# Optimization experiments

Measured on AMD Instinct MI355X. Metric: run time of the kernel, lower is better.

Reference implementation:

```python
import jax, jax.numpy as jnp
import numpy as np

M, N, E, B, J = 8192, 16384, 2097152, 8, 3
IMG, CH = 128, 1
BCLIP = 1.0  # rLayer B


def setup_inputs() -> dict:
    key = jax.random.key(0)
    ks = jax.random.split(key, 9)
    # ~E/M = 256 nnz per row -> scale vals so outputs stay O(1)
    A_vals = jax.random.normal(ks[0], (E,), jnp.float32) / 16.0
    A_rows = jax.random.randint(ks[1], (E,), 0, M, jnp.int32)
    A_cols = jax.random.randint(ks[2], (E,), 0, N, jnp.int32)
    z = jax.random.normal(ks[3], (B, N), jnp.float32)
    u = jax.random.normal(ks[4], (B, N), jnp.float32)
    y = jax.random.normal(ks[5], (B, M), jnp.float32)
    W1 = jax.random.normal(ks[6], (J, 3, 3, CH, 32), jnp.float32) * 0.05
    W2 = jax.random.normal(ks[7], (J, 3, 3, 32, 32), jnp.float32) * 0.05
    W3 = jax.random.normal(ks[8], (J, 3, 3, 32, CH), jnp.float32) * 0.05
    etas = jnp.full((J,), 1e-3, jnp.float32)
    return {"A_vals": A_vals, "A_rows": A_rows, "A_cols": A_cols,
            "z": z, "u": u, "y": y, "W1": W1, "W2": W2, "W3": W3, "etas": etas}


def _spmm_xAT(x, vals, rows, cols):
    """x (B,N) @ A^T -> (B,M), A in COO (rows in [0,M), cols in [0,N))."""
    contrib = x.T[cols] * vals[:, None]            # (E, B)
    return jax.ops.segment_sum(contrib, rows, num_segments=M).T


def _spmm_xA(x, vals, rows, cols):
    """x (B,M) @ A -> (B,N)."""
    contrib = x.T[rows] * vals[:, None]            # (E, B)
    return jax.ops.segment_sum(contrib, cols, num_segments=N).T


def _conv(x, w):
    return jax.lax.conv_general_dilated(
        x, w, window_strides=(1, 1), padding='SAME',
        dimension_numbers=('NHWC', 'HWIO', 'NHWC'))


def reference(A_vals, A_rows, A_cols, z, u, y, W1, W2, W3, etas):
    for j in range(J):
        # rLayer: ISTA gradient step with per-sample norm clipping (normalize=True)
        resid = y - _spmm_xAT(z * u, A_vals, A_rows, A_cols)      # (B, M)
        v = u * _spmm_xA(resid, A_vals, A_rows, A_cols)           # (B, N)
        v_norm = jnp.linalg.norm(v, axis=1, keepdims=True)        # (B, 1)
        v = v / jnp.maximum(1.0, v_norm / BCLIP)
        r = z - etas[j] * v
        # CNN prox: two relu convs + linear conv, no bias
        x = r.reshape(B, IMG, IMG, CH)
        x = jax.nn.relu(_conv(x, W1[j]))
        x = jax.nn.relu(_conv(x, W2[j]))
        x = _conv(x, W3[j])
        z = jax.nn.relu(r + x.reshape(B, N))                      # project=True
    return z
```

## Files before the change

### kernel.cpp

```cpp
#include <hip/hip_runtime.h>
#include <hip/hip_bf16.h>

#define Mdim 8192
#define Ndim 16384
#define Ennz 2097152
#define Bsz 8
#define Jit 3
#define IMG 128
#define RCAP 512
#define CCAP 256
#define PSTRIDE 270336
#define QSTRIDE 135168

typedef __attribute__((ext_vector_type(8))) short bf8_t;
typedef __attribute__((ext_vector_type(4))) float f4_t;

__device__ __forceinline__ short f2b(float f){
    __hip_bfloat16 h = __float2bfloat16(f);
    return *reinterpret_cast<short*>(&h);
}
__device__ __forceinline__ float bval(unsigned e){
    return __uint_as_float(e & 0xFFFF0000u);
}

__global__ void k_prep(const float* __restrict__ W2, const float* __restrict__ W3,
                       short* __restrict__ w2p, short* __restrict__ w3p,
                       int* bin_pos, int* cnts){
    int i = blockIdx.x*256 + threadIdx.x;
    if(i < 24) bin_pos[i] = 0;
    if(i < 24576) cnts[i] = 0;
    if(i < 27648){
        int j = i / 9216, idx = i - j*9216;
        int kk = idx >> 10, rem = idx & 1023;
        int ic = rem >> 5, oc = rem & 31;
        w2p[(size_t)j*11520 + (kk*32 + oc)*40 + ic] = f2b(W2[i]);
    }
    if(i < 864) w3p[i] = f2b(W3[i]);
}

__global__ __launch_bounds__(256) void k_part(const float* __restrict__ vals,
        const int* __restrict__ rows, const int* __restrict__ cols,
        int* bin_pos, uint2* __restrict__ Pst, uint2* __restrict__ Qst){
    __shared__ int cnt[24], off[24], gbase[24], start[24];
    __shared__ uint2 stage[4096];
    int t = threadIdx.x;
    if(t < 24) cnt[t] = 0;
    __syncthreads();
    int base = blockIdx.x * 2048;
    int r[8], c[8]; float v[8];
    #pragma unroll
    for(int k = 0; k < 8; k++){
        int e = base + k*256 + t;
        r[k] = rows[e]; c[k] = cols[e]; v[k] = vals[e];
        atomicAdd(&cnt[r[k] >> 10], 1);
        atomicAdd(&cnt[8 + (c[k] >> 10)], 1);
    }
    __syncthreads();
    if(t == 0){
        int s = 0;
        for(int q = 0; q < 8; q++){ start[q] = s; s += cnt[q]; }
        s = 2048;
        for(int q = 8; q < 24; q++){ start[q] = s; s += cnt[q]; }
    }
    if(t < 24) off[t] = 0;
    __syncthreads();
    if(t < 24) gbase[t] = atomicAdd(&bin_pos[t], cnt[t]);
    #pragma unroll
    for(int k = 0; k < 8; k++){
        int pb = r[k] >> 10;
        int p = atomicAdd(&off[pb], 1);
        stage[start[pb] + p] = make_uint2(((unsigned)(r[k] & 1023) << 14) | (unsigned)c[k],
                                          __float_as_uint(v[k]));
        int qb = 8 + (c[k] >> 10);
        int q = atomicAdd(&off[qb], 1);
        stage[start[qb] + q] = make_uint2(((unsigned)(c[k] & 1023) << 13) | (unsigned)r[k],
                                          __float_as_uint(v[k]));
    }
    __syncthreads();
    for(int q = 0; q < 8; q++){
        int len = cnt[q];
        uint2* dst = Pst + (size_t)q*PSTRIDE + gbase[q];
        for(int k = t; k < len; k += 256) dst[k] = stage[start[q] + k];
    }
    for(int q = 8; q < 24; q++){
        int len = cnt[q];
        uint2* dst = Qst + (size_t)(q-8)*QSTRIDE + gbase[q];
        for(int k = t; k < len; k += 256) dst[k] = stage[start[q] + k];
    }
}

__global__ __launch_bounds__(256) void k_scat(const uint2* __restrict__ Pst,
        const uint2* __restrict__ Qst, const int* __restrict__ bin_pos,
        int* row_cnt, int* col_cnt, unsigned* __restrict__ rp, unsigned* __restrict__ cp,
        const float* __restrict__ z_in, const float* __restrict__ u,
        float* __restrict__ z_cur, float* __restrict__ zu_T){
    __shared__ int cnt[1024], curs[1024];
    int t = threadIdx.x;
    int bid = blockIdx.x;
    if(bid >= 768){
        int i = (bid - 768)*256 + t;
        int n = i >> 3, b = i & 7;
        float z = z_in[b*Ndim + n];
        z_cur[b*Ndim + n] = z;
        zu_T[i] = z * u[b*Ndim + n];
        return;
    }
    if(bid < 256){
        int g = bid & 7, chunk = bid >> 3;
        int len = bin_pos[g];
        int s0 = (int)(((long long)chunk * len) >> 5);
        int s1 = (int)(((long long)(chunk+1) * len) >> 5);
        for(int i = t; i < 1024; i += 256) cnt[i] = 0;
        __syncthreads();
        const uint2* base = Pst + (size_t)g*PSTRIDE;
        for(int k = s0 + t; k < s1; k += 256)
            atomicAdd(&cnt[base[k].x >> 14], 1);
        __syncthreads();
        for(int i = t; i < 1024; i += 256)
            curs[i] = atomicAdd(&row_cnt[g*1024 + i], cnt[i]);
        __syncthreads();
        for(int k = s0 + t; k < s1; k += 256){
            uint2 e = base[k];
            int r_l = e.x >> 14;
            int slot = atomicAdd(&curs[r_l], 1);
            if(slot < RCAP)
                rp[(size_t)(g*1024 + r_l)*RCAP + slot] =
                    (((unsigned)(unsigned short)f2b(__uint_as_float(e.y))) << 16)
                    | (e.x & 0x3FFFu);
        }
    } else {
        int bc = bid - 256;
        int g = bc & 15, chunk = bc >> 4;
        int len = bin_pos[8 + g];
        int s0 = (int)(((long long)chunk * len) >> 5);
        int s1 = (int)(((long long)(chunk+1) * len) >> 5);
        for(int i = t; i < 1024; i += 256) cnt[i] = 0;
        __syncthreads();
        const uint2* base = Qst + (size_t)g*QSTRIDE;
        for(int k = s0 + t; k < s1; k += 256)
            atomicAdd(&cnt[base[k].x >> 13], 1);
        __syncthreads();
        for(int i = t; i < 1024; i += 256)
            curs[i] = atomicAdd(&col_cnt[g*1024 + i], cnt[i]);
        __syncthreads();
        for(int k = s0 + t; k < s1; k += 256){
            uint2 e = base[k];
            int c_l = e.x >> 13;
            int slot = atomicAdd(&curs[c_l], 1);
            if(slot < CCAP)
                cp[(size_t)(g*1024 + c_l)*CCAP + slot] =
                    (((unsigned)(unsigned short)f2b(__uint_as_float(e.y))) << 16)
                    | (e.x & 0x1FFFu);
        }
    }
}

__global__ void k_spmm1g(const unsigned* __restrict__ rp, const int* __restrict__ row_cnt,
                         const float* __restrict__ y, const float* __restrict__ zu_T,
                         float* __restrict__ resid_T, float* __restrict__ ssq){
    if(blockIdx.x == 0 && threadIdx.x < 8) ssq[threadIdx.x] = 0.f;
    int m = (blockIdx.x*256 + threadIdx.x) >> 6;
    int lane = threadIdx.x & 63;
    int n_nz = min(row_cnt[m], RCAP);
    int b = lane & 7, ks = lane >> 3;
    const unsigned* base = rp + (size_t)m*RCAP;
    float acc = 0.f;
    for(int k = ks*4; k < n_nz; k += 32){
        uint4 e = *(const uint4*)(base + k);
        float w0 = bval(e.x);
        float w1 = (k+1 < n_nz) ? bval(e.y) : 0.f;
        float w2 = (k+2 < n_nz) ? bval(e.z) : 0.f;
        float w3 = (k+3 < n_nz) ? bval(e.w) : 0.f;
        acc = fmaf(w0, zu_T[(e.x & 0x3FFFu)*8 + b], acc);
        acc = fmaf(w1, zu_T[(e.y & 0x3FFFu)*8 + b], acc);
        acc = fmaf(w2, zu_T[(e.z & 0x3FFFu)*8 + b], acc);
        acc = fmaf(w3, zu_T[(e.w & 0x3FFFu)*8 + b], acc);
    }
    acc += __shfl_xor(acc, 8);
    acc += __shfl_xor(acc, 16);
    acc += __shfl_xor(acc, 32);
    if(ks == 0)
        resid_T[m*8 + b] = y[b*Mdim + m] - acc;
}

__global__ void k_spmm2g(const unsigned* __restrict__ cp, const int* __restrict__ col_cnt,
                         const float* __restrict__ resid_T, float* __restrict__ v_T){
    int n = (blockIdx.x*256 + threadIdx.x) >> 6;
    int lane = threadIdx.x & 63;
    int n_nz = min(col_cnt[n], CCAP);
    int b = lane & 7, ks = lane >> 3;
    const unsigned* base = cp + (size_t)n*CCAP;
    float acc = 0.f;
    for(int k = ks*4; k < n_nz; k += 32){
        uint4 e = *(const uint4*)(base + k);
        float w0 = bval(e.x);
        float w1 = (k+1 < n_nz) ? bval(e.y) : 0.f;
        float w2 = (k+2 < n_nz) ? bval(e.z) : 0.f;
        float w3 = (k+3 < n_nz) ? bval(e.w) : 0.f;
        acc = fmaf(w0, resid_T[(e.x & 0x1FFFu)*8 + b], acc);
        acc = fmaf(w1, resid_T[(e.y & 0x1FFFu)*8 + b], acc);
        acc = fmaf(w2, resid_T[(e.z & 0x1FFFu)*8 + b], acc);
        acc = fmaf(w3, resid_T[(e.w & 0x1FFFu)*8 + b], acc);
    }
    acc += __shfl_xor(acc, 8);
    acc += __shfl_xor(acc, 16);
    acc += __shfl_xor(acc, 32);
    if(ks == 0)
        v_T[n*8 + b] = acc;
}

__global__ __launch_bounds__(256) void k_normp(const float* __restrict__ u,
                        const float* __restrict__ v_T, float* __restrict__ ssq){
    int t = threadIdx.x;
    float s = 0.f;
    #pragma unroll
    for(int c = 0; c < 4; c++){
        int idx = c*32768 + blockIdx.x*256 + t;
        int n = idx >> 3, b = idx & 7;
        float tv = u[b*Ndim + n] * v_T[idx];
        s = fmaf(tv, tv, s);
    }
    s += __shfl_xor(s, 8);
    s += __shfl_xor(s, 16);
    s += __shfl_xor(s, 32);
    if(((t & 63) >> 3) == 0) atomicAdd(&ssq[t & 7], s);
}

__global__ __launch_bounds__(256) void k_conv123(
        const float* __restrict__ z_cur, const float* __restrict__ u,
        const float* __restrict__ v_T, const float* __restrict__ ssq,
        const float* __restrict__ etas, const float* __restrict__ W1,
        const short* __restrict__ w2p, const short* __restrict__ w3p,
        int j, float* __restrict__ dst, float* __restrict__ zu_T){
    __shared__ short w2t[9*32*40];
    __shared__ short x1t[144*40];
    __shared__ short x2t[100*40];
    __shared__ float w1s[288];
    __shared__ short w3b[288];
    __shared__ float r14[196];
    int t = threadIdx.x;
    int blk = blockIdx.x;
    int bb = blk >> 8, tile = blk & 255;
    int oy0 = (tile >> 4)*8, ox0 = (tile & 15)*8;

    for(int idx = t; idx < 1440; idx += 256)
        ((uint4*)w2t)[idx] = ((const uint4*)(w2p + (size_t)j*11520))[idx];
    for(int idx = t; idx < 288; idx += 256){
        w1s[idx] = W1[j*288 + idx];
        w3b[idx] = w3p[j*288 + idx];
    }
    if(t < 196){
        int yy = t/14, xx = t%14;
        int gy = oy0 + yy - 3, gx = ox0 + xx - 3;
        float val = 0.f;
        if((unsigned)gy < 128u && (unsigned)gx < 128u){
            int n = gy*IMG + gx;
            int idx = bb*Ndim + n;
            float scale = etas[j] / fmaxf(1.0f, sqrtf(ssq[bb]));
            val = z_cur[idx] - scale * u[idx] * v_T[n*8 + bb];
        }
        r14[t] = val;
    }
    __syncthreads();

    for(int idx = t; idx < 2304; idx += 256){
        int ocp = idx & 15, p = idx >> 4;
        int py = p/12, px = p%12;
        int gy = oy0 + py - 2, gx = ox0 + px - 2;
        float a0 = 0.f, a1 = 0.f;
        if((unsigned)gy < 128u && (unsigned)gx < 128u){
            #pragma unroll
            for(int ky = 0; ky < 3; ky++)
                #pragma unroll
                for(int kx = 0; kx < 3; kx++){
                    float rv = r14[(py+ky)*14 + (px+kx)];
                    a0 = fmaf(rv, w1s[(ky*3+kx)*32 + 2*ocp],     a0);
                    a1 = fmaf(rv, w1s[(ky*3+kx)*32 + 2*ocp + 1], a1);
                }
            a0 = fmaxf(a0, 0.f); a1 = fmaxf(a1, 0.f);
        }
        unsigned pack = (unsigned short)f2b(a0) | ((unsigned)(unsigned short)f2b(a1) << 16);
        ((unsigned*)x1t)[p*20 + ocp] = pack;
    }
    __syncthreads();

    int wv = t >> 6, lane = t & 63, mm = lane & 15, q = lane >> 4;

    #pragma unroll
    for(int rnd = 0; rnd < 2; rnd++){
        int p = rnd*64 + wv*16 + mm;
        int pp = min(p, 99);
        int py2 = pp/10, px2 = pp%10;
        f4_t acc0 = {0.f,0.f,0.f,0.f}, acc1 = {0.f,0.f,0.f,0.f};
        #pragma unroll
        for(int kk = 0; kk < 9; kk++){
            int ky = kk/3, kx = kk%3;
            bf8_t a  = *(const bf8_t*)&x1t[((py2+ky)*12 + (px2+kx))*40 + q*8];
            bf8_t b0 = *(const bf8_t*)&w2t[(kk*32 + mm)*40 + q*8];
            bf8_t b1 = *(const bf8_t*)&w2t[(kk*32 + 16 + mm)*40 + q*8];
            acc0 = __builtin_amdgcn_mfma_f32_16x16x32_bf16(a, b0, acc0, 0, 0, 0);
            acc1 = __builtin_amdgcn_mfma_f32_16x16x32_bf16(a, b1, acc1, 0, 0, 0);
        }
        #pragma unroll
        for(int reg = 0; reg < 4; reg++){
            int pw = rnd*64 + wv*16 + q*4 + reg;
            if(pw < 100){
                int py = pw/10, px = pw%10;
                int gy = oy0 + py - 1, gx = ox0 + px - 1;
                bool in = ((unsigned)gy < 128u) && ((unsigned)gx < 128u);
                x2t[pw*40 + mm]      = in ? f2b(fmaxf(acc0[reg], 0.f)) : (short)0;
                x2t[pw*40 + mm + 16] = in ? f2b(fmaxf(acc1[reg], 0.f)) : (short)0;
            }
        }
    }
    __syncthreads();

    int p3 = wv*16 + mm;
    int py3 = p3 >> 3, px3 = p3 & 7;
    f4_t acc = {0.f,0.f,0.f,0.f};
    #pragma unroll
    for(int kk = 0; kk < 9; kk++){
        int ky = kk/3, kx = kk%3;
        bf8_t a = *(const bf8_t*)&x2t[((py3+ky)*10 + (px3+kx))*40 + q*8];
        bf8_t bf;
        #pragma unroll
        for(int jj = 0; jj < 8; jj++)
            bf[jj] = (mm == 0) ? w3b[kk*32 + q*8 + jj] : (short)0;
        acc = __builtin_amdgcn_mfma_f32_16x16x32_bf16(a, bf, acc, 0, 0, 0);
    }
    if(mm == 0){
        #pragma unroll
        for(int reg = 0; reg < 4; reg++){
            int po = wv*16 + q*4 + reg;
            int py = po >> 3, px = po & 7;
            int gy = oy0 + py, gx = ox0 + px;
            int n = gy*IMG + gx;
            int idx = bb*Ndim + n;
            float r = r14[(py+3)*14 + (px+3)];
            float znew = fmaxf(r + acc[reg], 0.f);
            dst[idx] = znew;
            zu_T[n*8 + bb] = znew * u[idx];
        }
    }
}

extern "C" void kernel_launch(void* const* d_in, const int* in_sizes, int n_in,
                              void* d_out, int out_size, void* d_ws, size_t ws_size,
                              hipStream_t stream){
    const float* A_vals = (const float*)d_in[0];
    const int* A_rows = (const int*)d_in[1];
    const int* A_cols = (const int*)d_in[2];
    const float* z_in = (const float*)d_in[3];
    const float* u    = (const float*)d_in[4];
    const float* y    = (const float*)d_in[5];
    const float* W1   = (const float*)d_in[6];
    const float* W2   = (const float*)d_in[7];
    const float* W3   = (const float*)d_in[8];
    const float* etas = (const float*)d_in[9];

    float* ws = (float*)d_ws;
    float* z_cur   = ws;  ws += Bsz*Ndim;
    float* zu_T    = ws;  ws += Ndim*8;
    float* v_T     = ws;  ws += Ndim*8;
    float* resid_T = ws;  ws += Mdim*8;
    float* ssq     = ws;  ws += 8;
    int*   bin_pos = (int*)ws; ws += 32;
    int*   row_cnt = (int*)ws; ws += Mdim;
    int*   col_cnt = (int*)ws; ws += Ndim;
    short* w2p     = (short*)ws; ws += 3*11520/2;
    short* w3p     = (short*)ws; ws += 3*288/2 + 8;
    unsigned* rp = (unsigned*)ws; ws += (size_t)Mdim*RCAP;
    unsigned* cp = (unsigned*)ws; ws += (size_t)Ndim*CCAP;
    uint2* Pst = (uint2*)ws;  ws += (size_t)8*PSTRIDE*2;
    uint2* Qst = (uint2*)ws;

    k_prep<<<108, 256, 0, stream>>>(W2, W3, w2p, w3p, bin_pos, row_cnt);
    k_part<<<Ennz/2048, 256, 0, stream>>>(A_vals, A_rows, A_cols, bin_pos, Pst, Qst);
    k_scat<<<1280, 256, 0, stream>>>(Pst, Qst, bin_pos, row_cnt, col_cnt, rp, cp,
                                     z_in, u, z_cur, zu_T);

    for(int j = 0; j < Jit; j++){
        k_spmm1g<<<Mdim/4, 256, 0, stream>>>(rp, row_cnt, y, zu_T, resid_T, ssq);
        k_spmm2g<<<Ndim/4, 256, 0, stream>>>(cp, col_cnt, resid_T, v_T);
        k_normp<<<128, 256, 0, stream>>>(u, v_T, ssq);
        float* dst = (j == Jit-1) ? (float*)d_out : z_cur;
        k_conv123<<<Bsz*256, 256, 0, stream>>>(z_cur, u, v_T, ssq, etas,
                                               W1, w2p, w3p, j, dst, zu_T);
    }
}
```

Before: 326.9 us.

## Fuse norm reduction into SpMM2 and loop conv tiles per block

The per-sample squared-norm reduction moves into the second SpMM kernel. Each block accumulates in LDS and atomically adds into 64 striped partial slots, which removes the separate k_normp launch and its reread of v_T. The conv kernel now processes 4 tiles per block (512 blocks instead of 2048), so the shared W2/W1/W3 weight staging and the partial-norm reduction are amortised across tiles. z is ping-ponged between two buffers so that reads of the source and writes of the next iterate never alias. The trade-off is fewer conv blocks, which may lower occupancy and latency hiding, and more contended LDS atomics in SpMM2.

```diff
diff --git a/kernel.cpp b/kernel.cpp
--- a/kernel.cpp
+++ b/kernel.cpp
@@ -157,8 +157,11 @@
 
 __global__ void k_spmm1g(const unsigned* __restrict__ rp, const int* __restrict__ row_cnt,
                          const float* __restrict__ y, const float* __restrict__ zu_T,
-                         float* __restrict__ resid_T, float* __restrict__ ssq){
-    if(blockIdx.x == 0 && threadIdx.x < 8) ssq[threadIdx.x] = 0.f;
+                         float* __restrict__ resid_T, float* __restrict__ ssq_part){
+    if(blockIdx.x == 0){
+        ssq_part[threadIdx.x] = 0.f;
+        ssq_part[256 + threadIdx.x] = 0.f;
+    }
     int m = (blockIdx.x*256 + threadIdx.x) >> 6;
     int lane = threadIdx.x & 63;
     int n_nz = min(row_cnt[m], RCAP);
@@ -184,9 +187,14 @@
 }
 
 __global__ void k_spmm2g(const unsigned* __restrict__ cp, const int* __restrict__ col_cnt,
-                         const float* __restrict__ resid_T, float* __restrict__ v_T){
-    int n = (blockIdx.x*256 + threadIdx.x) >> 6;
-    int lane = threadIdx.x & 63;
+                         const float* __restrict__ resid_T, const float* __restrict__ u,
+                         float* __restrict__ v_T, float* __restrict__ ssq_part){
+    __shared__ float sred[8];
+    int t = threadIdx.x;
+    if(t < 8) sred[t] = 0.f;
+    __syncthreads();
+    int n = (blockIdx.x*256 + t) >> 6;
+    int lane = t & 63;
     int n_nz = min(col_cnt[n], CCAP);
     int b = lane & 7, ks = lane >> 3;
     const unsigned* base = cp + (size_t)n*CCAP;
@@ -205,43 +213,31 @@
     acc += __shfl_xor(acc, 8);
     acc += __shfl_xor(acc, 16);
     acc += __shfl_xor(acc, 32);
-    if(ks == 0)
+    if(ks == 0){
         v_T[n*8 + b] = acc;
-}
-
-__global__ __launch_bounds__(256) void k_normp(const float* __restrict__ u,
-                        const float* __restrict__ v_T, float* __restrict__ ssq){
-    int t = threadIdx.x;
-    float s = 0.f;
-    #pragma unroll
-    for(int c = 0; c < 4; c++){
-        int idx = c*32768 + blockIdx.x*256 + t;
-        int n = idx >> 3, b = idx & 7;
-        float tv = u[b*Ndim + n] * v_T[idx];
-        s = fmaf(tv, tv, s);
-    }
-    s += __shfl_xor(s, 8);
-    s += __shfl_xor(s, 16);
-    s += __shfl_xor(s, 32);
-    if(((t & 63) >> 3) == 0) atomicAdd(&ssq[t & 7], s);
+        float uv = u[b*Ndim + n] * acc;
+        atomicAdd(&sred[b], uv*uv);
+    }
+    __syncthreads();
+    if(t < 8) atomicAdd(&ssq_part[(blockIdx.x & 63)*8 + t], sred[t]);
 }
 
 __global__ __launch_bounds__(256) void k_conv123(
-        const float* __restrict__ z_cur, const float* __restrict__ u,
-        const float* __restrict__ v_T, const float* __restrict__ ssq,
+        const float* __restrict__ z_src, const float* __restrict__ u,
+        const float* __restrict__ v_T, const float* __restrict__ ssq_part,
         const float* __restrict__ etas, const float* __restrict__ W1,
         const short* __restrict__ w2p, const short* __restrict__ w3p,
-        int j, float* __restrict__ dst, float* __restrict__ zu_T){
+        int j, float* __restrict__ z_dst, float* __restrict__ zu_T){
     __shared__ short w2t[9*32*40];
     __shared__ short x1t[144*40];
     __shared__ short x2t[100*40];
     __shared__ float w1s[288];
     __shared__ short w3b[288];
     __shared__ float r14[196];
+    __shared__ float sc_lds;
     int t = threadIdx.x;
     int blk = blockIdx.x;
-    int bb = blk >> 8, tile = blk & 255;
-    int oy0 = (tile >> 4)*8, ox0 = (tile & 15)*8;
+    int bb = blk >> 6, tgroup = blk & 63;
 
     for(int idx = t; idx < 1440; idx += 256)
         ((uint4*)w2t)[idx] = ((const uint4*)(w2p + (size_t)j*11520))[idx];
@@ -249,98 +245,112 @@
         w1s[idx] = W1[j*288 + idx];
         w3b[idx] = w3p[j*288 + idx];
     }
-    if(t < 196){
-        int yy = t/14, xx = t%14;
-        int gy = oy0 + yy - 3, gx = ox0 + xx - 3;
-        float val = 0.f;
-        if((unsigned)gy < 128u && (unsigned)gx < 128u){
-            int n = gy*IMG + gx;
-            int idx = bb*Ndim + n;
-            float scale = etas[j] / fmaxf(1.0f, sqrtf(ssq[bb]));
-            val = z_cur[idx] - scale * u[idx] * v_T[n*8 + bb];
-        }
-        r14[t] = val;
-    }
-    __syncthreads();
-
-    for(int idx = t; idx < 2304; idx += 256){
-        int ocp = idx & 15, p = idx >> 4;
-        int py = p/12, px = p%12;
-        int gy = oy0 + py - 2, gx = ox0 + px - 2;
-        float a0 = 0.f, a1 = 0.f;
-        if((unsigned)gy < 128u && (unsigned)gx < 128u){
+    if(t < 64){
+        float sv = ssq_part[t*8 + bb];
+        #pragma unroll
+        for(int off = 32; off > 0; off >>= 1) sv += __shfl_xor(sv, off);
+        if(t == 0) sc_lds = etas[j] / fmaxf(1.0f, sqrtf(sv));
+    }
+    __syncthreads();
+    float sc = sc_lds;
+
+    int wv = t >> 6, lane = t & 63, mm = lane & 15, q = lane >> 4;
+
+    for(int tt = 0; tt < 4; tt++){
+        int tile = tgroup*4 + tt;
+        int oy0 = (tile >> 4)*8, ox0 = (tile & 15)*8;
+
+        if(t < 196){
+            int yy = t/14, xx = t%14;
+            int gy = oy0 + yy - 3, gx = ox0 + xx - 3;
+            float val = 0.f;
+            if((unsigned)gy < 128u && (unsigned)gx < 128u){
+                int n = gy*IMG + gx;
+                int idx = bb*Ndim + n;
+                val = z_src[idx] - sc * u[idx] * v_T[n*8 + bb];
+            }
+            r14[t] = val;
+        }
+        __syncthreads();
+
+        for(int idx = t; idx < 2304; idx += 256){
+            int ocp = idx & 15, p = idx >> 4;
+            int py = p/12, px = p%12;
+            int gy = oy0 + py - 2, gx = ox0 + px - 2;
+            float a0 = 0.f, a1 = 0.f;
+            if((unsigned)gy < 128u && (unsigned)gx < 128u){
+                #pragma unroll
+                for(int ky = 0; ky < 3; ky++)
+                    #pragma unroll
+                    for(int kx = 0; kx < 3; kx++){
+                        float rv = r14[(py+ky)*14 + (px+kx)];
+                        a0 = fmaf(rv, w1s[(ky*3+kx)*32 + 2*ocp],     a0);
+                        a1 = fmaf(rv, w1s[(ky*3+kx)*32 + 2*ocp + 1], a1);
+                    }
+                a0 = fmaxf(a0, 0.f); a1 = fmaxf(a1, 0.f);
+            }
+            unsigned pack = (unsigned short)f2b(a0) | ((unsigned)(unsigned short)f2b(a1) << 16);
+            ((unsigned*)x1t)[p*20 + ocp] = pack;
+        }
+        __syncthreads();
+
+        #pragma unroll
+        for(int rnd = 0; rnd < 2; rnd++){
+            int p = rnd*64 + wv*16 + mm;
+            int pp = min(p, 99);
+            int py2 = pp/10, px2 = pp%10;
+            f4_t acc0 = {0.f,0.f,0.f,0.f}, acc1 = {0.f,0.f,0.f,0.f};
             #pragma unroll
-            for(int ky = 0; ky < 3; ky++)
-                #pragma unroll
-                for(int kx = 0; kx < 3; kx++){
-                    float rv = r14[(py+ky)*14 + (px+kx)];
-                    a0 = fmaf(rv, w1s[(ky*3+kx)*32 + 2*ocp],     a0);
-                    a1 = fmaf(rv, w1s[(ky*3+kx)*32 + 2*ocp + 1], a1);
+            for(int kk = 0; kk < 9; kk++){
+                int ky = kk/3, kx = kk%3;
+                bf8_t a  = *(const bf8_t*)&x1t[((py2+ky)*12 + (px2+kx))*40 + q*8];
+                bf8_t b0 = *(const bf8_t*)&w2t[(kk*32 + mm)*40 + q*8];
+                bf8_t b1 = *(const bf8_t*)&w2t[(kk*32 + 16 + mm)*40 + q*8];
+                acc0 = __builtin_amdgcn_mfma_f32_16x16x32_bf16(a, b0, acc0, 0, 0, 0);
+                acc1 = __builtin_amdgcn_mfma_f32_16x16x32_bf16(a, b1, acc1, 0, 0, 0);
+            }
+            #pragma unroll
+            for(int reg = 0; reg < 4; reg++){
+                int pw = rnd*64 + wv*16 + q*4 + reg;
+                if(pw < 100){
+                    int py = pw/10, px = pw%10;
+                    int gy = oy0 + py - 1, gx = ox0 + px - 1;
+                    bool in = ((unsigned)gy < 128u) && ((unsigned)gx < 128u);
+                    x2t[pw*40 + mm]      = in ? f2b(fmaxf(acc0[reg], 0.f)) : (short)0;
+                    x2t[pw*40 + mm + 16] = in ? f2b(fmaxf(acc1[reg], 0.f)) : (short)0;
                 }
-            a0 = fmaxf(a0, 0.f); a1 = fmaxf(a1, 0.f);
-        }
-        unsigned pack = (unsigned short)f2b(a0) | ((unsigned)(unsigned short)f2b(a1) << 16);
-        ((unsigned*)x1t)[p*20 + ocp] = pack;
-    }
-    __syncthreads();
-
-    int wv = t >> 6, lane = t & 63, mm = lane & 15, q = lane >> 4;
-
-    #pragma unroll
-    for(int rnd = 0; rnd < 2; rnd++){
-        int p = rnd*64 + wv*16 + mm;
-        int pp = min(p, 99);
-        int py2 = pp/10, px2 = pp%10;
-        f4_t acc0 = {0.f,0.f,0.f,0.f}, acc1 = {0.f,0.f,0.f,0.f};
+            }
+        }
+        __syncthreads();
+
+        int p3 = wv*16 + mm;
+        int py3 = p3 >> 3, px3 = p3 & 7;
+        f4_t acc = {0.f,0.f,0.f,0.f};
         #pragma unroll
         for(int kk = 0; kk < 9; kk++){
             int ky = kk/3, kx = kk%3;
-            bf8_t a  = *(const bf8_t*)&x1t[((py2+ky)*12 + (px2+kx))*40 + q*8];
-            bf8_t b0 = *(const bf8_t*)&w2t[(kk*32 + mm)*40 + q*8];
-            bf8_t b1 = *(const bf8_t*)&w2t[(kk*32 + 16 + mm)*40 + q*8];
-            acc0 = __builtin_amdgcn_mfma_f32_16x16x32_bf16(a, b0, acc0, 0, 0, 0);
-            acc1 = __builtin_amdgcn_mfma_f32_16x16x32_bf16(a, b1, acc1, 0, 0, 0);
-        }
-        #pragma unroll
-        for(int reg = 0; reg < 4; reg++){
-            int pw = rnd*64 + wv*16 + q*4 + reg;
-            if(pw < 100){
-                int py = pw/10, px = pw%10;
-                int gy = oy0 + py - 1, gx = ox0 + px - 1;
-                bool in = ((unsigned)gy < 128u) && ((unsigned)gx < 128u);
-                x2t[pw*40 + mm]      = in ? f2b(fmaxf(acc0[reg], 0.f)) : (short)0;
-                x2t[pw*40 + mm + 16] = in ? f2b(fmaxf(acc1[reg], 0.f)) : (short)0;
+            bf8_t a = *(const bf8_t*)&x2t[((py3+ky)*10 + (px3+kx))*40 + q*8];
+            bf8_t bf;
+            #pragma unroll
+            for(int jj = 0; jj < 8; jj++)
+                bf[jj] = (mm == 0) ? w3b[kk*32 + q*8 + jj] : (short)0;
+            acc = __builtin_amdgcn_mfma_f32_16x16x32_bf16(a, bf, acc, 0, 0, 0);
+        }
+        if(mm == 0){
+            #pragma unroll
+            for(int reg = 0; reg < 4; reg++){
+                int po = wv*16 + q*4 + reg;
+                int py = po >> 3, px = po & 7;
+                int gy = oy0 + py, gx = ox0 + px;
+                int n = gy*IMG + gx;
+                int idx = bb*Ndim + n;
+                float r = r14[(py+3)*14 + (px+3)];
+                float znew = fmaxf(r + acc[reg], 0.f);
+                z_dst[idx] = znew;
+                zu_T[n*8 + bb] = znew * u[idx];
             }
         }
-    }
-    __syncthreads();
-
-    int p3 = wv*16 + mm;
-    int py3 = p3 >> 3, px3 = p3 & 7;
-    f4_t acc = {0.f,0.f,0.f,0.f};
-    #pragma unroll
-    for(int kk = 0; kk < 9; kk++){
-        int ky = kk/3, kx = kk%3;
-        bf8_t a = *(const bf8_t*)&x2t[((py3+ky)*10 + (px3+kx))*40 + q*8];
-        bf8_t bf;
-        #pragma unroll
-        for(int jj = 0; jj < 8; jj++)
-            bf[jj] = (mm == 0) ? w3b[kk*32 + q*8 + jj] : (short)0;
-        acc = __builtin_amdgcn_mfma_f32_16x16x32_bf16(a, bf, acc, 0, 0, 0);
-    }
-    if(mm == 0){
-        #pragma unroll
-        for(int reg = 0; reg < 4; reg++){
-            int po = wv*16 + q*4 + reg;
-            int py = po >> 3, px = po & 7;
-            int gy = oy0 + py, gx = ox0 + px;
-            int n = gy*IMG + gx;
-            int idx = bb*Ndim + n;
-            float r = r14[(py+3)*14 + (px+3)];
-            float znew = fmaxf(r + acc[reg], 0.f);
-            dst[idx] = znew;
-            zu_T[n*8 + bb] = znew * u[idx];
-        }
+        __syncthreads();
     }
 }
 
@@ -359,11 +369,12 @@
     const float* etas = (const float*)d_in[9];
 
     float* ws = (float*)d_ws;
-    float* z_cur   = ws;  ws += Bsz*Ndim;
+    float* zA      = ws;  ws += Bsz*Ndim;
+    float* zB      = ws;  ws += Bsz*Ndim;
     float* zu_T    = ws;  ws += Ndim*8;
     float* v_T     = ws;  ws += Ndim*8;
     float* resid_T = ws;  ws += Mdim*8;
-    float* ssq     = ws;  ws += 8;
+    float* ssq_part= ws;  ws += 512;
     int*   bin_pos = (int*)ws; ws += 32;
     int*   row_cnt = (int*)ws; ws += Mdim;
     int*   col_cnt = (int*)ws; ws += Ndim;
@@ -377,14 +388,14 @@
     k_prep<<<108, 256, 0, stream>>>(W2, W3, w2p, w3p, bin_pos, row_cnt);
     k_part<<<Ennz/2048, 256, 0, stream>>>(A_vals, A_rows, A_cols, bin_pos, Pst, Qst);
     k_scat<<<1280, 256, 0, stream>>>(Pst, Qst, bin_pos, row_cnt, col_cnt, rp, cp,
-                                     z_in, u, z_cur, zu_T);
+                                     z_in, u, zA, zu_T);
 
     for(int j = 0; j < Jit; j++){
-        k_spmm1g<<<Mdim/4, 256, 0, stream>>>(rp, row_cnt, y, zu_T, resid_T, ssq);
-        k_spmm2g<<<Ndim/4, 256, 0, stream>>>(cp, col_cnt, resid_T, v_T);
-        k_normp<<<128, 256, 0, stream>>>(u, v_T, ssq);
-        float* dst = (j == Jit-1) ? (float*)d_out : z_cur;
-        k_conv123<<<Bsz*256, 256, 0, stream>>>(z_cur, u, v_T, ssq, etas,
-                                               W1, w2p, w3p, j, dst, zu_T);
-    }
-}
+        k_spmm1g<<<Mdim/4, 256, 0, stream>>>(rp, row_cnt, y, zu_T, resid_T, ssq_part);
+        k_spmm2g<<<Ndim/4, 256, 0, stream>>>(cp, col_cnt, resid_T, u, v_T, ssq_part);
+        const float* zsrc = (j & 1) ? zB : zA;
+        float* zdst = (j == Jit-1) ? (float*)d_out : ((j & 1) ? zA : zB);
+        k_conv123<<<512, 256, 0, stream>>>(zsrc, u, v_T, ssq_part, etas,
+                                           W1, w2p, w3p, j, zdst, zu_T);
+    }
+}
```

New measurement: 312.6 us. 1.05x faster.
